# Kernel optimization log

Hardware: AMD Instinct MI355X
Metric: run time of the kernel (lower is better)

The kernel has to match this reference:

```python
import jax, jax.numpy as jnp
import numpy as np
import math

D_MODEL = 1024
N_HEADS = 16
D_HEAD = D_MODEL // N_HEADS


def setup_inputs() -> dict:
    key = jax.random.key(0)
    ks = jax.random.split(key, 5)
    B, T, C = 4, 2048, D_MODEL
    s = 1.0 / math.sqrt(C)
    return {
        "x": jax.random.normal(ks[0], (B, T, C), dtype=jnp.float32),
        "qkv_w": jax.random.normal(ks[1], (3 * C, C), dtype=jnp.float32) * s,
        "qkv_b": jnp.zeros((3 * C,), dtype=jnp.float32),
        "out_w": jax.random.normal(ks[2], (C, C), dtype=jnp.float32) * s,
        "out_b": jnp.zeros((C,), dtype=jnp.float32),
    }


def reference(x, qkv_w, qkv_b, out_w, out_b):
    B, T, C = x.shape
    H, Dh = N_HEADS, D_HEAD
    qkv = x @ qkv_w.T + qkv_b              # [B,T,3C] (torch Linear: x W^T + b)
    q, k, v = jnp.split(qkv, 3, axis=-1)
    # [B,T,C] -> [B,H,T,Dh]
    q = q.reshape(B, T, H, Dh).transpose(0, 2, 1, 3)
    k = k.reshape(B, T, H, Dh).transpose(0, 2, 1, 3)
    v = v.reshape(B, T, H, Dh).transpose(0, 2, 1, 3)
    att = jnp.einsum("bhqd,bhkd->bhqk", q, k) / math.sqrt(Dh)
    causal = jnp.tril(jnp.ones((T, T), dtype=bool))  # True = keep
    att = jnp.where(causal, att, -jnp.inf)
    att = jax.nn.softmax(att, axis=-1)
    y = jnp.einsum("bhqk,bhkd->bhqd", att, v)
    y = y.transpose(0, 2, 1, 3).reshape(B, T, C)
    return y @ out_w.T + out_b
```

## Files before the change

### kernel.cpp

```cpp
#include <hip/hip_runtime.h>

typedef __attribute__((ext_vector_type(4))) float f32x4;
typedef __attribute__((ext_vector_type(16))) float f32x16;
typedef __attribute__((ext_vector_type(8))) __bf16 bf16x8;
typedef __attribute__((ext_vector_type(4))) __bf16 bf16x4;
typedef __attribute__((ext_vector_type(2))) unsigned u32x2;

#define MFMA_B16(a,b,c) __builtin_amdgcn_mfma_f32_16x16x32_bf16((a),(b),(c),0,0,0)
#define MFMA32(a,b,c)  __builtin_amdgcn_mfma_f32_32x32x16_bf16((a),(b),(c),0,0,0)

static constexpr int T_LEN  = 2048;
static constexpr int C_DIM  = 1024;
static constexpr int H_NUM  = 16;
static constexpr int D_HEADc = 64;
static constexpr float Q_PRESCALE = 0.125f * 1.4426950408889634f;

__device__ __forceinline__ void async16(const void* g, void* l) {
  __builtin_amdgcn_global_load_lds(
      (const __attribute__((address_space(1))) unsigned int*)g,
      (__attribute__((address_space(3))) unsigned int*)l, 16, 0, 0);
}

__device__ __forceinline__ unsigned cvtpk(float lo, float hi) {
  unsigned r;
  asm("v_cvt_pk_bf16_f32 %0, %1, %2" : "=v"(r) : "v"(lo), "v"(hi));
  return r;
}

__global__ __launch_bounds__(256) void cvt3_kernel(const float* __restrict__ a, __bf16* __restrict__ da, int na,
                                                   const float* __restrict__ b, __bf16* __restrict__ db, int nb,
                                                   const float* __restrict__ c, __bf16* __restrict__ dc, int nc) {
  int i = blockIdx.x * 256 + threadIdx.x;
  const float* s;
  __bf16* d;
  long j;
  if (i < na) { s = a; d = da; j = i; }
  else if (i < na + nb) { s = b; d = db; j = i - na; }
  else if (i < na + nb + nc) { s = c; d = dc; j = i - na - nb; }
  else return;
  float4 f = reinterpret_cast<const float4*>(s)[j];
  bf16x4 o;
  o.x = (__bf16)f.x; o.y = (__bf16)f.y; o.z = (__bf16)f.z; o.w = (__bf16)f.w;
  reinterpret_cast<bf16x4*>(d)[j] = o;
}

__global__ __launch_bounds__(256) void gemm_qkv(const __bf16* __restrict__ A,
                                                const __bf16* __restrict__ W,
                                                const float* __restrict__ bias,
                                                __bf16* __restrict__ qb,
                                                __bf16* __restrict__ kb,
                                                __bf16* __restrict__ vb) {
  constexpr int K = 1024;
  __shared__ __bf16 As[128 * 64];
  __shared__ __bf16 Bs[128 * 64];
  const int tid = threadIdx.x;
  const int wid = tid >> 6, lane = tid & 63, l16 = lane & 15, lg = lane >> 4;
  const int r8 = lane >> 3, sl = lane & 7;
  const int r7 = l16 & 7;
  const int wm = wid >> 1, wn = wid & 1;
  const int m0 = blockIdx.x * 128;

  for (int half = 0; half < 2; ++half) {
    const int n0 = blockIdx.y * 256 + half * 128;

    f32x4 acc[4][4];
#pragma unroll
    for (int i = 0; i < 4; ++i)
#pragma unroll
      for (int j = 0; j < 4; ++j) acc[i][j] = f32x4{0.f, 0.f, 0.f, 0.f};

    for (int k0 = 0; k0 < K; k0 += 64) {
      __builtin_amdgcn_s_barrier();
#pragma unroll
      for (int it = 0; it < 4; ++it) {
        int chunk = it * 4 + wid;
        int row = chunk * 8 + r8;
        int scol = ((sl ^ (row & 7)) << 3);
        async16(A + (long)(m0 + row) * K + k0 + scol, &As[chunk * 512]);
        async16(W + (long)(n0 + row) * K + k0 + scol, &Bs[chunk * 512]);
      }
      asm volatile("s_waitcnt vmcnt(0)" ::: "memory");
      __builtin_amdgcn_s_barrier();
#pragma unroll
      for (int kt = 0; kt < 2; ++kt) {
        const int sw = ((((kt << 2) | lg) ^ r7) << 3);
        bf16x8 af[4], bfv[4];
#pragma unroll
        for (int mi = 0; mi < 4; ++mi)
          af[mi] = *reinterpret_cast<const bf16x8*>(&As[(wm * 64 + mi * 16 + l16) * 64 + sw]);
#pragma unroll
        for (int nt = 0; nt < 4; ++nt)
          bfv[nt] = *reinterpret_cast<const bf16x8*>(&Bs[(wn * 64 + nt * 16 + l16) * 64 + sw]);
#pragma unroll
        for (int mi = 0; mi < 4; ++mi)
#pragma unroll
          for (int nt = 0; nt < 4; ++nt)
            acc[mi][nt] = MFMA_B16(af[mi], bfv[nt], acc[mi][nt]);
      }
    }

    const int which = n0 >> 10;
    if (which == 0) {
#pragma unroll
      for (int mi = 0; mi < 4; ++mi)
#pragma unroll
        for (int nt = 0; nt < 4; ++nt)
#pragma unroll
          for (int r = 0; r < 4; ++r) {
            int m = m0 + wm * 64 + mi * 16 + lg * 4 + r;
            int n = n0 + wn * 64 + nt * 16 + l16;
            int cc = n & 1023;
            int h = cc >> 6, d = cc & 63;
            long b = m >> 11, t = m & 2047;
            qb[(((b * H_NUM + h) * T_LEN) + t) * D_HEADc + d] =
                (__bf16)((acc[mi][nt][r] + bias[n]) * Q_PRESCALE);
          }
    } else if (which == 1) {
#pragma unroll
      for (int mi = 0; mi < 4; ++mi)
#pragma unroll
        for (int nt = 0; nt < 4; ++nt)
#pragma unroll
          for (int r = 0; r < 4; ++r) {
            int m = m0 + wm * 64 + mi * 16 + lg * 4 + r;
            int n = n0 + wn * 64 + nt * 16 + l16;
            int cc = n & 1023;
            int h = cc >> 6, d = cc & 63;
            long b = m >> 11, t = m & 2047;
            kb[(((b * H_NUM + h) * T_LEN) + t) * D_HEADc + d] = (__bf16)(acc[mi][nt][r] + bias[n]);
          }
    } else {
#pragma unroll
      for (int mi = 0; mi < 4; ++mi)
#pragma unroll
        for (int nt = 0; nt < 4; ++nt) {
          int n = n0 + wn * 64 + nt * 16 + l16;
          int cc = n & 1023;
          int h = cc >> 6, d = cc & 63;
          int t0 = m0 + wm * 64 + mi * 16 + lg * 4;
          long b = t0 >> 11;
          long t = t0 & 2047;
          float bv = bias[n];
          bf16x4 pk;
#pragma unroll
          for (int r = 0; r < 4; ++r) pk[r] = (__bf16)(acc[mi][nt][r] + bv);
          *reinterpret_cast<bf16x4*>(
              &vb[(((b * H_NUM + h) * D_HEADc) + d) * T_LEN + t]) = pk;
        }
    }
  }
}

__global__ __launch_bounds__(512, 4) void attn_kernel(const __bf16* __restrict__ q,
                                                      const __bf16* __restrict__ k,
                                                      const __bf16* __restrict__ vt,
                                                      __bf16* __restrict__ y) {
  __shared__ __bf16 Ks[2][2][64 * 64];
  __shared__ __bf16 Vs[2][2][64 * 64];
  const int tid = threadIdx.x;
  const int wid = tid >> 6, lane = tid & 63;
  const int l31 = lane & 31, hi = lane >> 5;
  const int r8 = lane >> 3, sl = lane & 7;
  const int r7 = l31 & 7;
  const int bid = blockIdx.x;
  const int qt = 15 - (bid >> 6);
  const int bh = bid & 63;
  const int grp = wid >> 2;
  const int wq = wid & 3;
  const int q0 = qt * 128;
  const int qw = q0 + wq * 32;
  const int qglob = qw + l31;
  const __bf16* qg = q + (long)bh * T_LEN * D_HEADc;
  const __bf16* kg = k + (long)bh * T_LEN * D_HEADc;
  const __bf16* vg = vt + (long)bh * T_LEN * D_HEADc;
  const long bb = bh >> 4;
  const int h = bh & 15;

  union { unsigned short us[8]; bf16x8 v; } ones_u;
#pragma unroll
  for (int i = 0; i < 8; ++i) ones_u.us[i] = 0x3F80;
  const bf16x8 ones = ones_u.v;

  f32x16 z16;
#pragma unroll
  for (int r = 0; r < 16; ++r) z16[r] = 0.f;

  bf16x8 qf[4];
#pragma unroll
  for (int dt = 0; dt < 4; ++dt)
    qf[dt] = *reinterpret_cast<const bf16x8*>(qg + (long)qglob * D_HEADc + dt * 16 + hi * 8);

  f32x16 o[2];
  o[0] = z16; o[1] = z16;
  f32x16 lacc = z16;

  auto stage = [&](int buf, int i) {
#pragma unroll
    for (int it = 0; it < 4; ++it) {
      int slot = it * 8 + wid;
      int g = slot & 7;
      int kind = slot >> 3;
      int par = kind >> 1, isv = kind & 1;
      int row = g * 8 + r8;
      int scol = ((sl ^ (row & 7)) << 3);
      int k0s = (2 * i + par) * 64;
      if (!isv)
        async16(kg + (long)(k0s + row) * D_HEADc + scol, &Ks[buf][par][g * 512]);
      else
        async16(vg + (long)row * T_LEN + k0s + scol, &Vs[buf][par][g * 512]);
    }
  };

  const int iters = qt + 1;
  stage(0, 0);
  int cur = 0;
  for (int i = 0; i < iters; ++i) {
    if (i + 1 < iters) {
      stage(cur ^ 1, i + 1);
      asm volatile("s_waitcnt vmcnt(4)" ::: "memory");
    } else {
      asm volatile("s_waitcnt vmcnt(0)" ::: "memory");
    }
    __builtin_amdgcn_s_barrier();
    const int k0 = (2 * i + grp) * 64;
    if (k0 < qw + 32) {
      const __bf16* Kc = Ks[cur][grp];
      const __bf16* Vc = Vs[cur][grp];
      f32x16 s[2];
      __builtin_amdgcn_s_setprio(1);
      {
        const int swz = (hi ^ r7) << 3;
        bf16x8 kf0 = *reinterpret_cast<const bf16x8*>(&Kc[l31 * 64 + swz]);
        bf16x8 kf1 = *reinterpret_cast<const bf16x8*>(&Kc[(32 + l31) * 64 + swz]);
        s[0] = MFMA32(kf0, qf[0], z16);
        s[1] = MFMA32(kf1, qf[0], z16);
      }
#pragma unroll
      for (int dt = 1; dt < 4; ++dt) {
        const int swz = (((dt << 1) | hi) ^ r7) << 3;
        bf16x8 kf0 = *reinterpret_cast<const bf16x8*>(&Kc[l31 * 64 + swz]);
        bf16x8 kf1 = *reinterpret_cast<const bf16x8*>(&Kc[(32 + l31) * 64 + swz]);
        s[0] = MFMA32(kf0, qf[dt], s[0]);
        s[1] = MFMA32(kf1, qf[dt], s[1]);
      }
      __builtin_amdgcn_s_setprio(0);

      if (k0 + 63 > qw) {
#pragma unroll
        for (int r = 0; r < 16; ++r) {
          const int kb = (r & 3) + 8 * (r >> 2) + 4 * hi;
          if (k0 + kb > qglob) s[0][r] = -3e38f;
          if (k0 + 32 + kb > qglob) s[1][r] = -3e38f;
        }
      }

#pragma unroll
      for (int ki = 0; ki < 2; ++ki)
#pragma unroll
        for (int r = 0; r < 16; ++r) s[ki][r] = exp2f(s[ki][r]);

      unsigned pb[4][4];
#pragma unroll
      for (int ki = 0; ki < 2; ++ki) {
        unsigned d0 = cvtpk(s[ki][0], s[ki][1]),   d1 = cvtpk(s[ki][2], s[ki][3]);
        unsigned d2 = cvtpk(s[ki][4], s[ki][5]),   d3 = cvtpk(s[ki][6], s[ki][7]);
        unsigned d4 = cvtpk(s[ki][8], s[ki][9]),   d5 = cvtpk(s[ki][10], s[ki][11]);
        unsigned d6 = cvtpk(s[ki][12], s[ki][13]), d7 = cvtpk(s[ki][14], s[ki][15]);
        u32x2 a2 = __builtin_amdgcn_permlane32_swap(d0, d2, false, false);
        u32x2 b2 = __builtin_amdgcn_permlane32_swap(d1, d3, false, false);
        pb[ki * 2][0] = a2[0]; pb[ki * 2][1] = b2[0];
        pb[ki * 2][2] = a2[1]; pb[ki * 2][3] = b2[1];
        u32x2 c2 = __builtin_amdgcn_permlane32_swap(d4, d6, false, false);
        u32x2 e2 = __builtin_amdgcn_permlane32_swap(d5, d7, false, false);
        pb[ki * 2 + 1][0] = c2[0]; pb[ki * 2 + 1][1] = e2[0];
        pb[ki * 2 + 1][2] = c2[1]; pb[ki * 2 + 1][3] = e2[1];
      }

      __builtin_amdgcn_s_setprio(1);
#pragma unroll
      for (int kt = 0; kt < 4; ++kt) {
        union { unsigned u[4]; bf16x8 v; } pu;
#pragma unroll
        for (int w = 0; w < 4; ++w) pu.u[w] = pb[kt][w];
        const int swz = (((kt << 1) | hi) ^ r7) << 3;
        bf16x8 vf0 = *reinterpret_cast<const bf16x8*>(&Vc[l31 * 64 + swz]);
        bf16x8 vf1 = *reinterpret_cast<const bf16x8*>(&Vc[(32 + l31) * 64 + swz]);
        o[0] = MFMA32(vf0, pu.v, o[0]);
        o[1] = MFMA32(vf1, pu.v, o[1]);
        lacc = MFMA32(ones, pu.v, lacc);
      }
      __builtin_amdgcn_s_setprio(0);
    }
    __builtin_amdgcn_s_barrier();
    cur ^= 1;
  }

  float* ob  = (float*)&Ks[0][0][0];
  float* lb  = (float*)&Vs[0][0][0];
  if (grp == 1) {
#pragma unroll
    for (int di = 0; di < 2; ++di)
#pragma unroll
      for (int r = 0; r < 16; ++r) {
        const int kb = (r & 3) + 8 * (r >> 2) + 4 * hi;
        ob[wq * 2048 + (di * 32 + kb) * 32 + l31] = o[di][r];
      }
    if (hi == 0) lb[wq * 32 + l31] = lacc[0];
  }
  __syncthreads();
  if (grp == 0) {
    const float inv = 1.f / (lacc[0] + lb[wq * 32 + l31]);
    const long row = bb * T_LEN + qglob;
#pragma unroll
    for (int di = 0; di < 2; ++di)
#pragma unroll
      for (int rr = 0; rr < 4; ++rr) {
        bf16x4 pk;
#pragma unroll
        for (int c = 0; c < 4; ++c) {
          const int r = rr * 4 + c;
          const int kb = rr * 8 + hi * 4 + c;
          float val = o[di][r] + ob[wq * 2048 + (di * 32 + kb) * 32 + l31];
          pk[c] = (__bf16)(val * inv);
        }
        *reinterpret_cast<bf16x4*>(
            &y[row * C_DIM + h * D_HEADc + di * 32 + rr * 8 + hi * 4]) = pk;
      }
  }
}

__global__ __launch_bounds__(256) void gemm_proj(const __bf16* __restrict__ A,
                                                 const __bf16* __restrict__ W,
                                                 const float* __restrict__ bias,
                                                 float* __restrict__ out) {
  constexpr int K = 1024;
  __shared__ __bf16 As[128 * 64];
  __shared__ __bf16 Bs[128 * 64];
  const int tid = threadIdx.x;
  const int wid = tid >> 6, lane = tid & 63, l16 = lane & 15, lg = lane >> 4;
  const int r8 = lane >> 3, sl = lane & 7;
  const int r7 = l16 & 7;
  const int wm = wid >> 1, wn = wid & 1;
  const int m0 = blockIdx.x * 128, n0 = blockIdx.y * 128;

  f32x4 acc[4][4];
#pragma unroll
  for (int i = 0; i < 4; ++i)
#pragma unroll
    for (int j = 0; j < 4; ++j) acc[i][j] = f32x4{0.f, 0.f, 0.f, 0.f};

  for (int k0 = 0; k0 < K; k0 += 64) {
    __builtin_amdgcn_s_barrier();
#pragma unroll
    for (int it = 0; it < 4; ++it) {
      int chunk = it * 4 + wid;
      int row = chunk * 8 + r8;
      int scol = ((sl ^ (row & 7)) << 3);
      async16(A + (long)(m0 + row) * K + k0 + scol, &As[chunk * 512]);
      async16(W + (long)(n0 + row) * K + k0 + scol, &Bs[chunk * 512]);
    }
    asm volatile("s_waitcnt vmcnt(0)" ::: "memory");
    __builtin_amdgcn_s_barrier();
#pragma unroll
    for (int kt = 0; kt < 2; ++kt) {
      const int sw = ((((kt << 2) | lg) ^ r7) << 3);
      bf16x8 af[4], bfv[4];
#pragma unroll
      for (int mi = 0; mi < 4; ++mi)
        af[mi] = *reinterpret_cast<const bf16x8*>(&As[(wm * 64 + mi * 16 + l16) * 64 + sw]);
#pragma unroll
      for (int nt = 0; nt < 4; ++nt)
        bfv[nt] = *reinterpret_cast<const bf16x8*>(&Bs[(wn * 64 + nt * 16 + l16) * 64 + sw]);
#pragma unroll
      for (int mi = 0; mi < 4; ++mi)
#pragma unroll
        for (int nt = 0; nt < 4; ++nt)
          acc[mi][nt] = MFMA_B16(af[mi], bfv[nt], acc[mi][nt]);
    }
  }
#pragma unroll
  for (int mi = 0; mi < 4; ++mi)
#pragma unroll
    for (int nt = 0; nt < 4; ++nt)
#pragma unroll
      for (int r = 0; r < 4; ++r) {
        long m = m0 + wm * 64 + mi * 16 + lg * 4 + r;
        int n = n0 + wn * 64 + nt * 16 + l16;
        out[m * C_DIM + n] = acc[mi][nt][r] + bias[n];
      }
}

extern "C" void kernel_launch(void* const* d_in, const int* in_sizes, int n_in,
                              void* d_out, int out_size, void* d_ws, size_t ws_size,
                              hipStream_t stream) {
  const float* x     = (const float*)d_in[0];
  const float* qkv_w = (const float*)d_in[1];
  const float* qkv_b = (const float*)d_in[2];
  const float* out_w = (const float*)d_in[3];
  const float* out_b = (const float*)d_in[4];
  float* out = (float*)d_out;

  const long NX  = 8192L * 1024;
  const long NWQ = 3072L * 1024;
  const long NWO = 1024L * 1024;
  const size_t need = (size_t)(5 * NX + NWQ + NWO) * 2;
  if (ws_size < need) return;

  __bf16* xb   = (__bf16*)d_ws;
  __bf16* wqkv = xb + NX;
  __bf16* wout = wqkv + NWQ;
  __bf16* qb   = wout + NWO;
  __bf16* kb   = qb + NX;
  __bf16* vb   = kb + NX;
  __bf16* yb   = vb + NX;

  const int na = (int)(NX / 4), nb = (int)(NWQ / 4), nc = (int)(NWO / 4);
  cvt3_kernel<<<(na + nb + nc + 255) / 256, 256, 0, stream>>>(x, xb, na, qkv_w, wqkv, nb, out_w, wout, nc);

  gemm_qkv<<<dim3(64, 12), 256, 0, stream>>>(xb, wqkv, qkv_b, qb, kb, vb);
  attn_kernel<<<dim3(1024), 512, 0, stream>>>(qb, kb, vb, yb);
  gemm_proj<<<dim3(64, 8), 256, 0, stream>>>(yb, wout, out_b, out);
}
```

Baseline: 179.5 us.

## Double-buffer LDS tiles in QKV and projection GEMMs, split QKV N-halves into blocks

Both GEMM kernels now use two LDS buffers and prefetch the next K-tile with async global-to-LDS loads while computing the current one, waiting only on the older batch. This hides global load latency behind the MFMA work. The QKV GEMM also drops its serial two-half loop, so each block handles 128 output columns and the grid doubles to 64x24 for more parallelism. The cost is twice the LDS per block, which may reduce occupancy, and an extra barrier per K iteration.

Measured after the change: 166.6 us, median of 3. 1.08x faster.

```diff
diff --git a/kernel.cpp b/kernel.cpp
--- a/kernel.cpp
+++ b/kernel.cpp
@@ -51,103 +51,111 @@
                                                 __bf16* __restrict__ kb,
                                                 __bf16* __restrict__ vb) {
   constexpr int K = 1024;
-  __shared__ __bf16 As[128 * 64];
-  __shared__ __bf16 Bs[128 * 64];
+  __shared__ __bf16 As[2][128 * 64];
+  __shared__ __bf16 Bs[2][128 * 64];
   const int tid = threadIdx.x;
   const int wid = tid >> 6, lane = tid & 63, l16 = lane & 15, lg = lane >> 4;
   const int r8 = lane >> 3, sl = lane & 7;
   const int r7 = l16 & 7;
   const int wm = wid >> 1, wn = wid & 1;
   const int m0 = blockIdx.x * 128;
-
-  for (int half = 0; half < 2; ++half) {
-    const int n0 = blockIdx.y * 256 + half * 128;
-
-    f32x4 acc[4][4];
-#pragma unroll
-    for (int i = 0; i < 4; ++i)
-#pragma unroll
-      for (int j = 0; j < 4; ++j) acc[i][j] = f32x4{0.f, 0.f, 0.f, 0.f};
-
-    for (int k0 = 0; k0 < K; k0 += 64) {
-      __builtin_amdgcn_s_barrier();
-#pragma unroll
-      for (int it = 0; it < 4; ++it) {
-        int chunk = it * 4 + wid;
-        int row = chunk * 8 + r8;
-        int scol = ((sl ^ (row & 7)) << 3);
-        async16(A + (long)(m0 + row) * K + k0 + scol, &As[chunk * 512]);
-        async16(W + (long)(n0 + row) * K + k0 + scol, &Bs[chunk * 512]);
-      }
+  const int n0 = blockIdx.y * 128;
+
+  f32x4 acc[4][4];
+#pragma unroll
+  for (int i = 0; i < 4; ++i)
+#pragma unroll
+    for (int j = 0; j < 4; ++j) acc[i][j] = f32x4{0.f, 0.f, 0.f, 0.f};
+
+  auto stageg = [&](int buf, int k0) {
+#pragma unroll
+    for (int it = 0; it < 4; ++it) {
+      int chunk = it * 4 + wid;
+      int row = chunk * 8 + r8;
+      int scol = ((sl ^ (row & 7)) << 3);
+      async16(A + (long)(m0 + row) * K + k0 + scol, &As[buf][chunk * 512]);
+      async16(W + (long)(n0 + row) * K + k0 + scol, &Bs[buf][chunk * 512]);
+    }
+  };
+
+  stageg(0, 0);
+  int cur = 0;
+  for (int k0 = 0; k0 < K; k0 += 64) {
+    if (k0 + 64 < K) {
+      stageg(cur ^ 1, k0 + 64);
+      asm volatile("s_waitcnt vmcnt(8)" ::: "memory");
+    } else {
       asm volatile("s_waitcnt vmcnt(0)" ::: "memory");
-      __builtin_amdgcn_s_barrier();
-#pragma unroll
-      for (int kt = 0; kt < 2; ++kt) {
-        const int sw = ((((kt << 2) | lg) ^ r7) << 3);
-        bf16x8 af[4], bfv[4];
-#pragma unroll
-        for (int mi = 0; mi < 4; ++mi)
-          af[mi] = *reinterpret_cast<const bf16x8*>(&As[(wm * 64 + mi * 16 + l16) * 64 + sw]);
+    }
+    __builtin_amdgcn_s_barrier();
+#pragma unroll
+    for (int kt = 0; kt < 2; ++kt) {
+      const int sw = ((((kt << 2) | lg) ^ r7) << 3);
+      bf16x8 af[4], bfv[4];
+#pragma unroll
+      for (int mi = 0; mi < 4; ++mi)
+        af[mi] = *reinterpret_cast<const bf16x8*>(&As[cur][(wm * 64 + mi * 16 + l16) * 64 + sw]);
+#pragma unroll
+      for (int nt = 0; nt < 4; ++nt)
+        bfv[nt] = *reinterpret_cast<const bf16x8*>(&Bs[cur][(wn * 64 + nt * 16 + l16) * 64 + sw]);
+#pragma unroll
+      for (int mi = 0; mi < 4; ++mi)
 #pragma unroll
         for (int nt = 0; nt < 4; ++nt)
-          bfv[nt] = *reinterpret_cast<const bf16x8*>(&Bs[(wn * 64 + nt * 16 + l16) * 64 + sw]);
-#pragma unroll
-        for (int mi = 0; mi < 4; ++mi)
-#pragma unroll
-          for (int nt = 0; nt < 4; ++nt)
-            acc[mi][nt] = MFMA_B16(af[mi], bfv[nt], acc[mi][nt]);
-      }
-    }
-
-    const int which = n0 >> 10;
-    if (which == 0) {
-#pragma unroll
-      for (int mi = 0; mi < 4; ++mi)
-#pragma unroll
-        for (int nt = 0; nt < 4; ++nt)
-#pragma unroll
-          for (int r = 0; r < 4; ++r) {
-            int m = m0 + wm * 64 + mi * 16 + lg * 4 + r;
-            int n = n0 + wn * 64 + nt * 16 + l16;
-            int cc = n & 1023;
-            int h = cc >> 6, d = cc & 63;
-            long b = m >> 11, t = m & 2047;
-            qb[(((b * H_NUM + h) * T_LEN) + t) * D_HEADc + d] =
-                (__bf16)((acc[mi][nt][r] + bias[n]) * Q_PRESCALE);
-          }
-    } else if (which == 1) {
-#pragma unroll
-      for (int mi = 0; mi < 4; ++mi)
-#pragma unroll
-        for (int nt = 0; nt < 4; ++nt)
-#pragma unroll
-          for (int r = 0; r < 4; ++r) {
-            int m = m0 + wm * 64 + mi * 16 + lg * 4 + r;
-            int n = n0 + wn * 64 + nt * 16 + l16;
-            int cc = n & 1023;
-            int h = cc >> 6, d = cc & 63;
-            long b = m >> 11, t = m & 2047;
-            kb[(((b * H_NUM + h) * T_LEN) + t) * D_HEADc + d] = (__bf16)(acc[mi][nt][r] + bias[n]);
-          }
-    } else {
-#pragma unroll
-      for (int mi = 0; mi < 4; ++mi)
-#pragma unroll
-        for (int nt = 0; nt < 4; ++nt) {
+          acc[mi][nt] = MFMA_B16(af[mi], bfv[nt], acc[mi][nt]);
+    }
+    __builtin_amdgcn_s_barrier();
+    cur ^= 1;
+  }
+
+  const int which = n0 >> 10;
+  if (which == 0) {
+#pragma unroll
+    for (int mi = 0; mi < 4; ++mi)
+#pragma unroll
+      for (int nt = 0; nt < 4; ++nt)
+#pragma unroll
+        for (int r = 0; r < 4; ++r) {
+          int m = m0 + wm * 64 + mi * 16 + lg * 4 + r;
           int n = n0 + wn * 64 + nt * 16 + l16;
           int cc = n & 1023;
           int h = cc >> 6, d = cc & 63;
-          int t0 = m0 + wm * 64 + mi * 16 + lg * 4;
-          long b = t0 >> 11;
-          long t = t0 & 2047;
-          float bv = bias[n];
-          bf16x4 pk;
-#pragma unroll
-          for (int r = 0; r < 4; ++r) pk[r] = (__bf16)(acc[mi][nt][r] + bv);
-          *reinterpret_cast<bf16x4*>(
-              &vb[(((b * H_NUM + h) * D_HEADc) + d) * T_LEN + t]) = pk;
+          long b = m >> 11, t = m & 2047;
+          qb[(((b * H_NUM + h) * T_LEN) + t) * D_HEADc + d] =
+              (__bf16)((acc[mi][nt][r] + bias[n]) * Q_PRESCALE);
         }
-    }
+  } else if (which == 1) {
+#pragma unroll
+    for (int mi = 0; mi < 4; ++mi)
+#pragma unroll
+      for (int nt = 0; nt < 4; ++nt)
+#pragma unroll
+        for (int r = 0; r < 4; ++r) {
+          int m = m0 + wm * 64 + mi * 16 + lg * 4 + r;
+          int n = n0 + wn * 64 + nt * 16 + l16;
+          int cc = n & 1023;
+          int h = cc >> 6, d = cc & 63;
+          long b = m >> 11, t = m & 2047;
+          kb[(((b * H_NUM + h) * T_LEN) + t) * D_HEADc + d] = (__bf16)(acc[mi][nt][r] + bias[n]);
+        }
+  } else {
+#pragma unroll
+    for (int mi = 0; mi < 4; ++mi)
+#pragma unroll
+      for (int nt = 0; nt < 4; ++nt) {
+        int n = n0 + wn * 64 + nt * 16 + l16;
+        int cc = n & 1023;
+        int h = cc >> 6, d = cc & 63;
+        int t0 = m0 + wm * 64 + mi * 16 + lg * 4;
+        long b = t0 >> 11;
+        long t = t0 & 2047;
+        float bv = bias[n];
+        bf16x4 pk;
+#pragma unroll
+        for (int r = 0; r < 4; ++r) pk[r] = (__bf16)(acc[mi][nt][r] + bv);
+        *reinterpret_cast<bf16x4*>(
+            &vb[(((b * H_NUM + h) * D_HEADc) + d) * T_LEN + t]) = pk;
+      }
   }
 }
 
@@ -334,8 +342,8 @@
                                                  const float* __restrict__ bias,
                                                  float* __restrict__ out) {
   constexpr int K = 1024;
-  __shared__ __bf16 As[128 * 64];
-  __shared__ __bf16 Bs[128 * 64];
+  __shared__ __bf16 As[2][128 * 64];
+  __shared__ __bf16 Bs[2][128 * 64];
   const int tid = threadIdx.x;
   const int wid = tid >> 6, lane = tid & 63, l16 = lane & 15, lg = lane >> 4;
   const int r8 = lane >> 3, sl = lane & 7;
@@ -349,17 +357,26 @@
 #pragma unroll
     for (int j = 0; j < 4; ++j) acc[i][j] = f32x4{0.f, 0.f, 0.f, 0.f};
 
-  for (int k0 = 0; k0 < K; k0 += 64) {
-    __builtin_amdgcn_s_barrier();
+  auto stageg = [&](int buf, int k0) {
 #pragma unroll
     for (int it = 0; it < 4; ++it) {
       int chunk = it * 4 + wid;
       int row = chunk * 8 + r8;
       int scol = ((sl ^ (row & 7)) << 3);
-      async16(A + (long)(m0 + row) * K + k0 + scol, &As[chunk * 512]);
-      async16(W + (long)(n0 + row) * K + k0 + scol, &Bs[chunk * 512]);
-    }
-    asm volatile("s_waitcnt vmcnt(0)" ::: "memory");
+      async16(A + (long)(m0 + row) * K + k0 + scol, &As[buf][chunk * 512]);
+      async16(W + (long)(n0 + row) * K + k0 + scol, &Bs[buf][chunk * 512]);
+    }
+  };
+
+  stageg(0, 0);
+  int cur = 0;
+  for (int k0 = 0; k0 < K; k0 += 64) {
+    if (k0 + 64 < K) {
+      stageg(cur ^ 1, k0 + 64);
+      asm volatile("s_waitcnt vmcnt(8)" ::: "memory");
+    } else {
+      asm volatile("s_waitcnt vmcnt(0)" ::: "memory");
+    }
     __builtin_amdgcn_s_barrier();
 #pragma unroll
     for (int kt = 0; kt < 2; ++kt) {
@@ -367,16 +384,18 @@
       bf16x8 af[4], bfv[4];
 #pragma unroll
       for (int mi = 0; mi < 4; ++mi)
-        af[mi] = *reinterpret_cast<const bf16x8*>(&As[(wm * 64 + mi * 16 + l16) * 64 + sw]);
+        af[mi] = *reinterpret_cast<const bf16x8*>(&As[cur][(wm * 64 + mi * 16 + l16) * 64 + sw]);
 #pragma unroll
       for (int nt = 0; nt < 4; ++nt)
-        bfv[nt] = *reinterpret_cast<const bf16x8*>(&Bs[(wn * 64 + nt * 16 + l16) * 64 + sw]);
+        bfv[nt] = *reinterpret_cast<const bf16x8*>(&Bs[cur][(wn * 64 + nt * 16 + l16) * 64 + sw]);
 #pragma unroll
       for (int mi = 0; mi < 4; ++mi)
 #pragma unroll
         for (int nt = 0; nt < 4; ++nt)
           acc[mi][nt] = MFMA_B16(af[mi], bfv[nt], acc[mi][nt]);
     }
+    __builtin_amdgcn_s_barrier();
+    cur ^= 1;
   }
 #pragma unroll
   for (int mi = 0; mi < 4; ++mi)
@@ -417,7 +436,7 @@
   const int na = (int)(NX / 4), nb = (int)(NWQ / 4), nc = (int)(NWO / 4);
   cvt3_kernel<<<(na + nb + nc + 255) / 256, 256, 0, stream>>>(x, xb, na, qkv_w, wqkv, nb, out_w, wout, nc);
 
-  gemm_qkv<<<dim3(64, 12), 256, 0, stream>>>(xb, wqkv, qkv_b, qb, kb, vb);
+  gemm_qkv<<<dim3(64, 24), 256, 0, stream>>>(xb, wqkv, qkv_b, qb, kb, vb);
   attn_kernel<<<dim3(1024), 512, 0, stream>>>(qb, kb, vb, yb);
   gemm_proj<<<dim3(64, 8), 256, 0, stream>>>(yb, wout, out_b, out);
 }
```
